# Performance work log

Hardware: AMD Instinct MI355X
Metric: run time of the kernel (lower is better)

## Reference

```python
import jax, jax.numpy as jnp
import numpy as np
import math

D_MODEL = 1024
N_HEAD = 16
D_K = D_MODEL // N_HEAD
THETA = 10000.0


def apply_rope(x, pos):
    # x: [b, h, s, d_k], pos: [b, s] int
    half = x.shape[-1] // 2
    inv_freq = THETA ** (-jnp.arange(half, dtype=jnp.float32) * 2.0 / x.shape[-1])  # [half]
    angles = pos[:, None, :, None].astype(jnp.float32) * inv_freq  # [b,1,s,half]
    cos, sin = jnp.cos(angles), jnp.sin(angles)
    x1, x2 = x[..., 0::2], x[..., 1::2]
    out_even = x1 * cos - x2 * sin
    out_odd = x1 * sin + x2 * cos
    # interleave back
    out = jnp.stack([out_even, out_odd], axis=-1).reshape(x.shape)
    return out


def setup_inputs() -> dict:
    key = jax.random.key(0)
    ks = jax.random.split(key, 10)
    b, s = 2, 2048
    x = jax.random.normal(ks[0], (b, s, D_MODEL), dtype=jnp.float32)
    token_position = jnp.broadcast_to(jnp.arange(s, dtype=jnp.int32), (b, s))
    scale = 0.02
    Wq = jax.random.normal(ks[1], (D_MODEL, D_MODEL), dtype=jnp.float32) * scale
    bq = jnp.zeros((D_MODEL,), dtype=jnp.float32)
    Wk = jax.random.normal(ks[2], (D_MODEL, D_MODEL), dtype=jnp.float32) * scale
    bk = jnp.zeros((D_MODEL,), dtype=jnp.float32)
    Wv = jax.random.normal(ks[3], (D_MODEL, D_MODEL), dtype=jnp.float32) * scale
    bv = jnp.zeros((D_MODEL,), dtype=jnp.float32)
    Wo = jax.random.normal(ks[4], (D_MODEL, D_MODEL), dtype=jnp.float32) * scale
    bo = jnp.zeros((D_MODEL,), dtype=jnp.float32)
    return {"x": x, "Wq": Wq, "bq": bq, "Wk": Wk, "bk": bk, "Wv": Wv, "bv": bv,
            "Wo": Wo, "bo": bo, "token_position": token_position}


def reference(x, Wq, bq, Wk, bk, Wv, bv, Wo, bo, token_position):
    b, s, d = x.shape
    h, dk = N_HEAD, D_K

    def proj(W, bias):
        y = jnp.einsum('bsd,ed->bse', x, W) + bias  # nn.Linear: x @ W.T + b
        return y.reshape(b, s, h, dk).transpose(0, 2, 1, 3)  # [b,h,s,dk]

    q = apply_rope(proj(Wq, bq), token_position)
    k = apply_rope(proj(Wk, bk), token_position)
    v = proj(Wv, bv)

    scores = jnp.einsum('bhnd,bhmd->bhnm', q, k) / math.sqrt(dk)
    causal = jnp.tril(jnp.ones((s, s), dtype=bool))
    scores = jnp.where(causal, scores, -jnp.inf)
    probs = jax.nn.softmax(scores, axis=-1)  # stable softmax
    attn = jnp.einsum('bhnm,bhmd->bhnd', probs, v)
    attn = attn.transpose(0, 2, 1, 3).reshape(b, s, d)
    return jnp.einsum('bsd,ed->bse', attn, Wo) + bo
```

## Files before the change

### kernel.cpp

```cpp
#include <hip/hip_runtime.h>
#include <math.h>

#define S_LEN 2048
#define DM 1024
#define NH 16
#define DK 64

typedef short s8v __attribute__((ext_vector_type(8)));
typedef float f4v __attribute__((ext_vector_type(4)));

__device__ inline ushort bf16_rn(float v) {
    unsigned u = __float_as_uint(v);
    u += 0x7FFFu + ((u >> 16) & 1u);
    return (ushort)(u >> 16);
}
__device__ inline float bf16f(ushort h) { return __uint_as_float(((unsigned)h) << 16); }

__global__ __launch_bounds__(256) void convert_kernel(
    const float* __restrict__ x,
    const float* __restrict__ Wq, const float* __restrict__ Wk,
    const float* __restrict__ Wv, const float* __restrict__ Wo,
    ushort* __restrict__ xh, ushort* __restrict__ xl,
    ushort* __restrict__ wh, ushort* __restrict__ wl)
{
    long idx = (long)blockIdx.x * 256 + threadIdx.x;
    const float4* src;
    ushort* dh; ushort* dl; long off;
    if (idx < 1048576) {
        src = (const float4*)x; off = idx; dh = xh; dl = xl;
    } else {
        long wi = idx - 1048576;
        int which = (int)(wi >> 18);
        const float* wp = which == 0 ? Wq : which == 1 ? Wk : which == 2 ? Wv : Wo;
        src = (const float4*)wp; off = wi & 262143;
        dh = wh + (long)which * 1048576;
        dl = wl + (long)which * 1048576;
    }
    float4 v = src[off];
    ushort4 hv, lv;
    hv.x = bf16_rn(v.x); lv.x = bf16_rn(v.x - bf16f(hv.x));
    hv.y = bf16_rn(v.y); lv.y = bf16_rn(v.y - bf16f(hv.y));
    hv.z = bf16_rn(v.z); lv.z = bf16_rn(v.z - bf16f(hv.z));
    hv.w = bf16_rn(v.w); lv.w = bf16_rn(v.w - bf16f(hv.w));
    ((ushort4*)dh)[off] = hv;
    ((ushort4*)dl)[off] = lv;
}

__global__ __launch_bounds__(256) void rope_table_kernel(float* __restrict__ tab) {
    int idx = blockIdx.x * 256 + threadIdx.x;
    if (idx >= S_LEN * 32) return;
    int p = idx >> 5, i = idx & 31;
    float invf = powf(10000.0f, -(float)(2 * i) / 64.0f);
    float ang = (float)p * invf;
    tab[idx * 2 + 0] = cosf(ang);
    tab[idx * 2 + 1] = sinf(ang);
}

template <int MODE>
__global__ __launch_bounds__(256, 2) void mfma_gemm(
    const ushort* __restrict__ Ah_g, const ushort* __restrict__ Al_g,
    const ushort* __restrict__ Wh_g, const ushort* __restrict__ Wl_g,
    const float* __restrict__ b0, const float* __restrict__ b1, const float* __restrict__ b2,
    const float* __restrict__ rope_tab, const int* __restrict__ tokpos,
    ushort* __restrict__ qh, ushort* __restrict__ ql,
    ushort* __restrict__ kh, ushort* __restrict__ kl,
    ushort* __restrict__ vh, ushort* __restrict__ vl,
    float* __restrict__ out)
{
    const int m0 = blockIdx.x * 128;
    const int n0 = blockIdx.y * 64;
    const int which = (MODE == 0) ? blockIdx.z : 0;
    const ushort* WhP = Wh_g + (long)(MODE == 0 ? which : 3) * 1048576;
    const ushort* WlP = Wl_g + (long)(MODE == 0 ? which : 3) * 1048576;
    const float* bias = (which == 0) ? b0 : (which == 1) ? b1 : b2;

    __shared__ ushort Ah[128 * 64], Al[128 * 64];
    __shared__ ushort Bh[64 * 64],  Bl[64 * 64];

    const int t = threadIdx.x;
    const int w = t >> 6, l = t & 63, g = l >> 4, c = l & 15;
    const int wm = w >> 1, wn = w & 1;

    const int rA2 = t >> 1;
    const int kh0 = (t & 1) * 32;
    const int rW  = t >> 2;
    const int kq0 = (t & 3) * 16;

    f4v acc[4][2];
#pragma unroll
    for (int i = 0; i < 4; ++i)
#pragma unroll
        for (int j = 0; j < 2; ++j) acc[i][j] = (f4v){0.f, 0.f, 0.f, 0.f};

    const ushort* ApH = Ah_g + (long)(m0 + rA2) * DM + kh0;
    const ushort* ApL = Al_g + (long)(m0 + rA2) * DM + kh0;
    const ushort* WpH = WhP + (long)(n0 + rW) * DM + kq0;
    const ushort* WpL = WlP + (long)(n0 + rW) * DM + kq0;

    s8v pah[4], pal[4], pwh[2], pwl[2];
#pragma unroll
    for (int q = 0; q < 4; ++q) {
        pah[q] = *(const s8v*)(ApH + q * 8);
        pal[q] = *(const s8v*)(ApL + q * 8);
    }
#pragma unroll
    for (int q = 0; q < 2; ++q) {
        pwh[q] = *(const s8v*)(WpH + q * 8);
        pwl[q] = *(const s8v*)(WpL + q * 8);
    }

    for (int ch = 0; ch < 16; ++ch) {
        __syncthreads();
#pragma unroll
        for (int q = 0; q < 4; ++q) {
            const int b = (kh0 >> 3) + q;
            const int sb = (b ^ (rA2 & 7)) * 8;
            *(s8v*)&Ah[rA2 * 64 + sb] = pah[q];
            *(s8v*)&Al[rA2 * 64 + sb] = pal[q];
        }
#pragma unroll
        for (int q = 0; q < 2; ++q) {
            const int b = (kq0 >> 3) + q;
            const int sb = (b ^ (rW & 7)) * 8;
            *(s8v*)&Bh[rW * 64 + sb] = pwh[q];
            *(s8v*)&Bl[rW * 64 + sb] = pwl[q];
        }
        __syncthreads();

        if (ch + 1 < 16) {
            const int k0 = (ch + 1) * 64;
#pragma unroll
            for (int q = 0; q < 4; ++q) {
                pah[q] = *(const s8v*)(ApH + k0 + q * 8);
                pal[q] = *(const s8v*)(ApL + k0 + q * 8);
            }
#pragma unroll
            for (int q = 0; q < 2; ++q) {
                pwh[q] = *(const s8v*)(WpH + k0 + q * 8);
                pwl[q] = *(const s8v*)(WpL + k0 + q * 8);
            }
        }

#pragma unroll
        for (int kc = 0; kc < 2; ++kc) {
            const int blk = ((kc * 4 + g) ^ (c & 7)) * 8;
            s8v afh[4], afl[4], bfh[2], bfl[2];
#pragma unroll
            for (int mf = 0; mf < 4; ++mf) {
                const int row = wm * 64 + mf * 16 + c;
                afh[mf] = *(const s8v*)&Ah[row * 64 + blk];
                afl[mf] = *(const s8v*)&Al[row * 64 + blk];
            }
#pragma unroll
            for (int nf = 0; nf < 2; ++nf) {
                const int row = wn * 32 + nf * 16 + c;
                bfh[nf] = *(const s8v*)&Bh[row * 64 + blk];
                bfl[nf] = *(const s8v*)&Bl[row * 64 + blk];
            }
#pragma unroll
            for (int mf = 0; mf < 4; ++mf)
#pragma unroll
                for (int nf = 0; nf < 2; ++nf) {
                    acc[mf][nf] = __builtin_amdgcn_mfma_f32_16x16x32_bf16(afh[mf], bfh[nf], acc[mf][nf], 0, 0, 0);
                    acc[mf][nf] = __builtin_amdgcn_mfma_f32_16x16x32_bf16(afh[mf], bfl[nf], acc[mf][nf], 0, 0, 0);
                    acc[mf][nf] = __builtin_amdgcn_mfma_f32_16x16x32_bf16(afl[mf], bfh[nf], acc[mf][nf], 0, 0, 0);
                }
        }
    }

#pragma unroll
    for (int nf = 0; nf < 2; ++nf) {
        const int ecol = n0 + wn * 32 + nf * 16 + c;
        const float bv = bias[ecol];
        if (MODE == 1) {
#pragma unroll
            for (int mf = 0; mf < 4; ++mf)
#pragma unroll
                for (int r = 0; r < 4; ++r) {
                    const int m = m0 + wm * 64 + mf * 16 + 4 * g + r;
                    out[(long)m * DM + ecol] = acc[mf][nf][r] + bv;
                }
        } else {
            const int hH = ecol >> 6, dk = ecol & 63, fi = dk >> 1;
            ushort* dh = (which == 0) ? qh : (which == 1) ? kh : vh;
            ushort* dl = (which == 0) ? ql : (which == 1) ? kl : vl;
#pragma unroll
            for (int mf = 0; mf < 4; ++mf)
#pragma unroll
                for (int r = 0; r < 4; ++r) {
                    const int m = m0 + wm * 64 + mf * 16 + 4 * g + r;
                    const float val = acc[mf][nf][r] + bv;
                    const float par = __shfl_xor(val, 1);
                    float vr;
                    if (which == 2) {
                        vr = val;
                    } else {
                        const int pos = tokpos[m];
                        const float2 cs = ((const float2*)rope_tab)[pos * 32 + fi];
                        vr = (c & 1) ? fmaf(par, cs.y, val * cs.x)
                                     : fmaf(val, cs.x, -par * cs.y);
                    }
                    const ushort hh = bf16_rn(vr);
                    const ushort ll = bf16_rn(vr - bf16f(hh));
                    const long base = ((long)((m >> 11) * NH + hH) * S_LEN + (m & (S_LEN - 1))) * DK + dk;
                    dh[base] = hh;
                    dl[base] = ll;
                }
        }
    }
}

__global__ __launch_bounds__(256, 2) void flash_kernel(
    const ushort* __restrict__ qh_g, const ushort* __restrict__ ql_g,
    const ushort* __restrict__ kh_g, const ushort* __restrict__ kl_g,
    const ushort* __restrict__ vh_g, const ushort* __restrict__ vl_g,
    ushort* __restrict__ ah_g, ushort* __restrict__ al_g)
{
    const int bh = blockIdx.y;
    const int qb = 15 - (int)blockIdx.x;
    const int t = threadIdx.x;
    const int w = t >> 6, l = t & 63, g = l >> 4, c = l & 15;
    const int h = bh & (NH - 1), b_idx = bh >> 4;
    const int q0w = qb * 128 + w * 32;

    __shared__ ushort Kh[64 * 64], Kl[64 * 64];
    __shared__ ushort Vh[64 * 64], Vl[64 * 64];
    __shared__ uint P_[8192];
    uint* Pw = P_ + (w * 2) * 1024;

    s8v qhf[2][2], qlf[2][2];
#pragma unroll
    for (int qf = 0; qf < 2; ++qf)
#pragma unroll
        for (int kc = 0; kc < 2; ++kc) {
            const long base = ((long)bh * S_LEN + q0w + qf * 16 + c) * DK + kc * 32 + g * 8;
            qhf[qf][kc] = *(const s8v*)(qh_g + base);
            qlf[qf][kc] = *(const s8v*)(ql_g + base);
        }

    f4v o[2][4];
#pragma unroll
    for (int qf = 0; qf < 2; ++qf)
#pragma unroll
        for (int nt = 0; nt < 4; ++nt) o[qf][nt] = (f4v){0.f, 0.f, 0.f, 0.f};
    float m_[2] = {-INFINITY, -INFINITY};
    float l_[2] = {0.f, 0.f};

    const int ntiles = 2 * qb + 2;

    s8v pkh[2], pkl[2], pvh[2], pvl[2];
    {
        const long rb = ((long)bh * S_LEN + l) * DK;
#pragma unroll
        for (int ib = 0; ib < 2; ++ib) {
            const int b = w + ib * 4;
            pkh[ib] = *(const s8v*)(kh_g + rb + b * 8);
            pkl[ib] = *(const s8v*)(kl_g + rb + b * 8);
            pvh[ib] = *(const s8v*)(vh_g + rb + b * 8);
            pvl[ib] = *(const s8v*)(vl_g + rb + b * 8);
        }
    }

    for (int tile = 0; tile < ntiles; ++tile) {
        __syncthreads();

#pragma unroll
        for (int ib = 0; ib < 2; ++ib) {
            const int b = w + ib * 4;
            const int sb = b ^ (l & 7);
            *(s8v*)&Kh[l * 64 + sb * 8] = pkh[ib];
            *(s8v*)&Kl[l * 64 + sb * 8] = pkl[ib];

            uint4 uh = *(uint4*)&pvh[ib];
            uint4 ul = *(uint4*)&pvl[ib];
            uint4 ph_, pl_;
            ph_.x = (uint)__shfl_xor((int)uh.x, 1); ph_.y = (uint)__shfl_xor((int)uh.y, 1);
            ph_.z = (uint)__shfl_xor((int)uh.z, 1); ph_.w = (uint)__shfl_xor((int)uh.w, 1);
            pl_.x = (uint)__shfl_xor((int)ul.x, 1); pl_.y = (uint)__shfl_xor((int)ul.y, 1);
            pl_.z = (uint)__shfl_xor((int)ul.z, 1); pl_.w = (uint)__shfl_xor((int)ul.w, 1);
            const int colp = l & ~1;
            const int odd  = l & 1;
#pragma unroll
            for (int j = 0; j < 4; ++j) {
                const ushort oj   = ((const ushort*)&uh)[j];
                const ushort oj4  = ((const ushort*)&uh)[j + 4];
                const ushort pj   = ((const ushort*)&ph_)[j];
                const ushort pj4  = ((const ushort*)&ph_)[j + 4];
                const ushort loj  = ((const ushort*)&ul)[j];
                const ushort loj4 = ((const ushort*)&ul)[j + 4];
                const ushort plj  = ((const ushort*)&pl_)[j];
                const ushort plj4 = ((const ushort*)&pl_)[j + 4];
                const int d   = b * 8 + (odd ? 4 + j : j);
                const uint hv = odd ? ((uint)pj4  | ((uint)oj4  << 16))
                                    : ((uint)oj   | ((uint)pj   << 16));
                const uint lv = odd ? ((uint)plj4 | ((uint)loj4 << 16))
                                    : ((uint)loj  | ((uint)plj  << 16));
                const int sc2 = (colp >> 3) ^ (d & 7);
                *(uint*)&Vh[d * 64 + sc2 * 8 + (colp & 7)] = hv;
                *(uint*)&Vl[d * 64 + sc2 * 8 + (colp & 7)] = lv;
            }
        }
        __syncthreads();

        if (tile + 1 < ntiles) {
            const long rb = ((long)bh * S_LEN + (tile + 1) * 64 + l) * DK;
#pragma unroll
            for (int ib = 0; ib < 2; ++ib) {
                const int b = w + ib * 4;
                pkh[ib] = *(const s8v*)(kh_g + rb + b * 8);
                pkl[ib] = *(const s8v*)(kl_g + rb + b * 8);
                pvh[ib] = *(const s8v*)(vh_g + rb + b * 8);
                pvl[ib] = *(const s8v*)(vl_g + rb + b * 8);
            }
        }

        const int kvbase = tile * 64;
        int nt_hi[2];
#pragma unroll
        for (int qf = 0; qf < 2; ++qf) {
            const int lim = q0w + qf * 16 + 15 - kvbase;
            int v = lim < 0 ? 0 : (lim >> 4) + 1;
            nt_hi[qf] = v > 4 ? 4 : v;
        }
        const bool dz = (kvbase + 63) > q0w;

        f4v sc[2][4];
#pragma unroll
        for (int qf = 0; qf < 2; ++qf)
#pragma unroll
            for (int nt = 0; nt < 4; ++nt) sc[qf][nt] = (f4v){0.f, 0.f, 0.f, 0.f};
#pragma unroll
        for (int nt = 0; nt < 4; ++nt) {
            if (nt >= nt_hi[1]) continue;
            const int kvl = nt * 16 + c;
#pragma unroll
            for (int kc = 0; kc < 2; ++kc) {
                const int blk = ((kc * 4 + g) ^ (c & 7)) * 8;
                s8v kfh = *(const s8v*)&Kh[kvl * 64 + blk];
                s8v kfl = *(const s8v*)&Kl[kvl * 64 + blk];
#pragma unroll
                for (int qf = 0; qf < 2; ++qf) {
                    if (nt >= nt_hi[qf]) continue;
                    sc[qf][nt] = __builtin_amdgcn_mfma_f32_16x16x32_bf16(kfh, qhf[qf][kc], sc[qf][nt], 0, 0, 0);
                    sc[qf][nt] = __builtin_amdgcn_mfma_f32_16x16x32_bf16(kfh, qlf[qf][kc], sc[qf][nt], 0, 0, 0);
                    sc[qf][nt] = __builtin_amdgcn_mfma_f32_16x16x32_bf16(kfl, qhf[qf][kc], sc[qf][nt], 0, 0, 0);
                }
            }
        }

#pragma unroll
        for (int qf = 0; qf < 2; ++qf) {
            if (nt_hi[qf] == 0) continue;
            float s_[4][4];
#pragma unroll
            for (int nt = 0; nt < 4; ++nt)
#pragma unroll
                for (int r = 0; r < 4; ++r) {
                    const float v = sc[qf][nt][r] * 0.125f;
                    const bool bad = (nt >= nt_hi[qf]) ||
                        (dz && (kvbase + 16 * nt + 4 * g + r > q0w + qf * 16 + c));
                    s_[nt][r] = bad ? -INFINITY : v;
                }
            float tm = -INFINITY;
#pragma unroll
            for (int nt = 0; nt < 4; ++nt)
#pragma unroll
                for (int r = 0; r < 4; ++r) tm = fmaxf(tm, s_[nt][r]);
            tm = fmaxf(tm, __shfl_xor(tm, 16));
            tm = fmaxf(tm, __shfl_xor(tm, 32));
            const float mnew = fmaxf(m_[qf], tm);
            const float corr = __expf(m_[qf] - mnew);
            uint* Pq = Pw + qf * 1024 + c * 64;
            float psum = 0.f;
#pragma unroll
            for (int nt = 0; nt < 4; ++nt) {
                const float p0 = __expf(s_[nt][0] - mnew);
                const float p1 = __expf(s_[nt][1] - mnew);
                const float p2 = __expf(s_[nt][2] - mnew);
                const float p3 = __expf(s_[nt][3] - mnew);
                psum += (p0 + p1) + (p2 + p3);
                const ushort h0 = bf16_rn(p0), h1 = bf16_rn(p1);
                const ushort h2 = bf16_rn(p2), h3 = bf16_rn(p3);
                const ushort e0 = bf16_rn(p0 - bf16f(h0)), e1 = bf16_rn(p1 - bf16f(h1));
                const ushort e2 = bf16_rn(p2 - bf16f(h2)), e3 = bf16_rn(p3 - bf16f(h3));
                const int u0 = ((2 * nt + (g >> 1)) ^ (c & 7)) * 4 + 2 * (g & 1);
                uint2 hw; hw.x = (uint)h0 | ((uint)h1 << 16); hw.y = (uint)h2 | ((uint)h3 << 16);
                uint2 lw; lw.x = (uint)e0 | ((uint)e1 << 16); lw.y = (uint)e2 | ((uint)e3 << 16);
                *(uint2*)(Pq + u0) = hw;
                *(uint2*)(Pq + 32 + u0) = lw;
            }
            psum += __shfl_xor(psum, 16);
            psum += __shfl_xor(psum, 32);
            l_[qf] = l_[qf] * corr + psum;
            m_[qf] = mnew;
            float cD0 = __shfl(corr, (l & 48) + 4 * g + 0);
            float cD1 = __shfl(corr, (l & 48) + 4 * g + 1);
            float cD2 = __shfl(corr, (l & 48) + 4 * g + 2);
            float cD3 = __shfl(corr, (l & 48) + 4 * g + 3);
#pragma unroll
            for (int nt = 0; nt < 4; ++nt) {
                o[qf][nt][0] *= cD0; o[qf][nt][1] *= cD1;
                o[qf][nt][2] *= cD2; o[qf][nt][3] *= cD3;
            }
        }

#pragma unroll
        for (int kc = 0; kc < 2; ++kc) {
            if (nt_hi[1] <= kc * 2) continue;
            const bool q0go = nt_hi[0] > kc * 2;
            const int pswz = ((4 * kc + g) ^ (c & 7)) * 4;
            s8v pa1h = *(const s8v*)(Pw + 1024 + c * 64 + pswz);
            s8v pa1l = *(const s8v*)(Pw + 1024 + c * 64 + 32 + pswz);
            s8v pa0h, pa0l;
            if (q0go) {
                pa0h = *(const s8v*)(Pw + c * 64 + pswz);
                pa0l = *(const s8v*)(Pw + c * 64 + 32 + pswz);
            }
#pragma unroll
            for (int nt = 0; nt < 4; ++nt) {
                const int dcol = nt * 16 + c;
                const int vblk = ((kc * 4 + g) ^ (c & 7)) * 8;
                s8v vfh = *(const s8v*)&Vh[dcol * 64 + vblk];
                s8v vfl = *(const s8v*)&Vl[dcol * 64 + vblk];
                o[1][nt] = __builtin_amdgcn_mfma_f32_16x16x32_bf16(pa1h, vfh, o[1][nt], 0, 0, 0);
                o[1][nt] = __builtin_amdgcn_mfma_f32_16x16x32_bf16(pa1h, vfl, o[1][nt], 0, 0, 0);
                o[1][nt] = __builtin_amdgcn_mfma_f32_16x16x32_bf16(pa1l, vfh, o[1][nt], 0, 0, 0);
                if (q0go) {
                    o[0][nt] = __builtin_amdgcn_mfma_f32_16x16x32_bf16(pa0h, vfh, o[0][nt], 0, 0, 0);
                    o[0][nt] = __builtin_amdgcn_mfma_f32_16x16x32_bf16(pa0h, vfl, o[0][nt], 0, 0, 0);
                    o[0][nt] = __builtin_amdgcn_mfma_f32_16x16x32_bf16(pa0l, vfh, o[0][nt], 0, 0, 0);
                }
            }
        }
    }

#pragma unroll
    for (int qf = 0; qf < 2; ++qf) {
        const float inv = 1.0f / l_[qf];
        float iD0 = __shfl(inv, (l & 48) + 4 * g + 0);
        float iD1 = __shfl(inv, (l & 48) + 4 * g + 1);
        float iD2 = __shfl(inv, (l & 48) + 4 * g + 2);
        float iD3 = __shfl(inv, (l & 48) + 4 * g + 3);
#pragma unroll
        for (int nt = 0; nt < 4; ++nt) {
            float v0 = o[qf][nt][0] * iD0;
            float v1 = o[qf][nt][1] * iD1;
            float v2 = o[qf][nt][2] * iD2;
            float v3 = o[qf][nt][3] * iD3;
            const long row0 = (long)b_idx * S_LEN + q0w + qf * 16 + 4 * g;
            const long col = h * DK + nt * 16 + c;
            float vv[4] = {v0, v1, v2, v3};
#pragma unroll
            for (int r = 0; r < 4; ++r) {
                const ushort hh = bf16_rn(vv[r]);
                const ushort ll = bf16_rn(vv[r] - bf16f(hh));
                ah_g[(row0 + r) * DM + col] = hh;
                al_g[(row0 + r) * DM + col] = ll;
            }
        }
    }
}

extern "C" void kernel_launch(void* const* d_in, const int* in_sizes, int n_in,
                              void* d_out, int out_size, void* d_ws, size_t ws_size,
                              hipStream_t stream) {
    const float* x   = (const float*)d_in[0];
    const float* Wq  = (const float*)d_in[1];
    const float* bq  = (const float*)d_in[2];
    const float* Wk  = (const float*)d_in[3];
    const float* bk  = (const float*)d_in[4];
    const float* Wv  = (const float*)d_in[5];
    const float* bv  = (const float*)d_in[6];
    const float* Wo  = (const float*)d_in[7];
    const float* bo  = (const float*)d_in[8];
    const int* tokpos = (const int*)d_in[9];
    float* out = (float*)d_out;

    char* wsb = (char*)d_ws;
    const long NE = 4194304;
    ushort* qh = (ushort*)wsb;
    ushort* ql = qh + NE;
    ushort* kh = ql + NE;
    ushort* kl = kh + NE;
    ushort* vh = kl + NE;
    ushort* vl = vh + NE;
    ushort* wh = (ushort*)(wsb + 48ll * 1024 * 1024);
    ushort* wl = (ushort*)(wsb + 56ll * 1024 * 1024);
    ushort* xh = (ushort*)(wsb + 64ll * 1024 * 1024);
    ushort* xl = (ushort*)(wsb + 72ll * 1024 * 1024);
    float* rope_tab = (float*)(wsb + 80ll * 1024 * 1024);

    convert_kernel<<<8192, 256, 0, stream>>>(x, Wq, Wk, Wv, Wo, xh, xl, wh, wl);
    rope_table_kernel<<<256, 256, 0, stream>>>(rope_tab);

    mfma_gemm<0><<<dim3(32, 16, 3), 256, 0, stream>>>(
        xh, xl, wh, wl, bq, bk, bv, rope_tab, tokpos,
        qh, ql, kh, kl, vh, vl, nullptr);

    flash_kernel<<<dim3(16, 32), 256, 0, stream>>>(
        qh, ql, kh, kl, vh, vl, xh, xl);

    mfma_gemm<1><<<dim3(32, 16, 1), 256, 0, stream>>>(
        xh, xl, wh, wl, bo, nullptr, nullptr, rope_tab, tokpos,
        nullptr, nullptr, nullptr, nullptr, nullptr, nullptr, out);
}
```

Baseline: 389.6 us.

## Pair low and high causal query blocks per workgroup for load balance

Each flash-attention workgroup now handles two 16-row query fragments per wave, one from a low query block and one from the mirrored high block, split into halves across adjacent blockIdx.x. This evens out causal work across workgroups, which were previously imbalanced because late query blocks iterate over many more KV tiles. The causal mask condition is now evaluated per fragment. The KV loop still runs to the high block's tile count, so the low fragment sits idle for most tiles and MFMA work per iteration drops on those tiles.

```diff
diff --git a/kernel.cpp b/kernel.cpp
--- a/kernel.cpp
+++ b/kernel.cpp
@@ -1,4 +1,5 @@
 #include <hip/hip_runtime.h>
+#include <hip/hip_bf16.h>
 #include <math.h>
 
 #define S_LEN 2048
@@ -217,11 +218,18 @@
     ushort* __restrict__ ah_g, ushort* __restrict__ al_g)
 {
     const int bh = blockIdx.y;
-    const int qb = 15 - (int)blockIdx.x;
+    const int p_ = (int)blockIdx.x >> 1;
+    const int half = (int)blockIdx.x & 1;
+    const int qb_hi = 15 - p_;
+    const int qb_lo = p_;
     const int t = threadIdx.x;
     const int w = t >> 6, l = t & 63, g = l >> 4, c = l & 15;
     const int h = bh & (NH - 1), b_idx = bh >> 4;
-    const int q0w = qb * 128 + w * 32;
+
+    int qbase[2];
+    qbase[0] = qb_lo * 128 + half * 64 + w * 16;
+    qbase[1] = qb_hi * 128 + half * 64 + w * 16;
+    const int ntiles = 2 * qb_hi + half + 1;
 
     __shared__ ushort Kh[64 * 64], Kl[64 * 64];
     __shared__ ushort Vh[64 * 64], Vl[64 * 64];
@@ -233,7 +241,7 @@
     for (int qf = 0; qf < 2; ++qf)
 #pragma unroll
         for (int kc = 0; kc < 2; ++kc) {
-            const long base = ((long)bh * S_LEN + q0w + qf * 16 + c) * DK + kc * 32 + g * 8;
+            const long base = ((long)bh * S_LEN + qbase[qf] + c) * DK + kc * 32 + g * 8;
             qhf[qf][kc] = *(const s8v*)(qh_g + base);
             qlf[qf][kc] = *(const s8v*)(ql_g + base);
         }
@@ -245,8 +253,6 @@
         for (int nt = 0; nt < 4; ++nt) o[qf][nt] = (f4v){0.f, 0.f, 0.f, 0.f};
     float m_[2] = {-INFINITY, -INFINITY};
     float l_[2] = {0.f, 0.f};
-
-    const int ntiles = 2 * qb + 2;
 
     s8v pkh[2], pkl[2], pvh[2], pvl[2];
     {
@@ -318,11 +324,10 @@
         int nt_hi[2];
 #pragma unroll
         for (int qf = 0; qf < 2; ++qf) {
-            const int lim = q0w + qf * 16 + 15 - kvbase;
+            const int lim = qbase[qf] + 15 - kvbase;
             int v = lim < 0 ? 0 : (lim >> 4) + 1;
             nt_hi[qf] = v > 4 ? 4 : v;
         }
-        const bool dz = (kvbase + 63) > q0w;
 
         f4v sc[2][4];
 #pragma unroll
@@ -351,6 +356,7 @@
 #pragma unroll
         for (int qf = 0; qf < 2; ++qf) {
             if (nt_hi[qf] == 0) continue;
+            const bool needMask = (kvbase + 63) > qbase[qf];
             float s_[4][4];
 #pragma unroll
             for (int nt = 0; nt < 4; ++nt)
@@ -358,7 +364,7 @@
                 for (int r = 0; r < 4; ++r) {
                     const float v = sc[qf][nt][r] * 0.125f;
                     const bool bad = (nt >= nt_hi[qf]) ||
-                        (dz && (kvbase + 16 * nt + 4 * g + r > q0w + qf * 16 + c));
+                        (needMask && (kvbase + 16 * nt + 4 * g + r > qbase[qf] + c));
                     s_[nt][r] = bad ? -INFINITY : v;
                 }
             float tm = -INFINITY;
@@ -443,13 +449,13 @@
         float iD3 = __shfl(inv, (l & 48) + 4 * g + 3);
 #pragma unroll
         for (int nt = 0; nt < 4; ++nt) {
-            float v0 = o[qf][nt][0] * iD0;
-            float v1 = o[qf][nt][1] * iD1;
-            float v2 = o[qf][nt][2] * iD2;
-            float v3 = o[qf][nt][3] * iD3;
-            const long row0 = (long)b_idx * S_LEN + q0w + qf * 16 + 4 * g;
+            float vv[4];
+            vv[0] = o[qf][nt][0] * iD0;
+            vv[1] = o[qf][nt][1] * iD1;
+            vv[2] = o[qf][nt][2] * iD2;
+            vv[3] = o[qf][nt][3] * iD3;
+            const long row0 = (long)b_idx * S_LEN + qbase[qf] + 4 * g;
             const long col = h * DK + nt * 16 + c;
-            float vv[4] = {v0, v1, v2, v3};
 #pragma unroll
             for (int r = 0; r < 4; ++r) {
                 const ushort hh = bf16_rn(vv[r]);
```

Result: faster. 341.6 us (-12.3%).
